# Kernel optimization log

Measured on AMD Instinct MI355X. Metric: run time of the kernel, lower is better.

The kernel has to match this reference:

```python
import jax, jax.numpy as jnp
import numpy as np

B, N, M, H, NH = 8, 1024, 512, 1024, 4
DH = H // NH          # 256 main attention head size
CDH = (H // 4) // 4   # 64  cross attention qk head size
EPS = 1e-12


def _ln(x, g, b):
    mu = jnp.mean(x, axis=-1, keepdims=True)
    var = jnp.mean((x - mu) ** 2, axis=-1, keepdims=True)
    return (x - mu) / jnp.sqrt(var + EPS) * g + b


def _heads(x, nh):
    b, n, d = x.shape
    return x.reshape(b, n, nh, d // nh).transpose(0, 2, 1, 3)  # [b,nh,n,dh]


def setup_inputs() -> dict:
    key = jax.random.key(0)
    ks = iter(jax.random.split(key, 64))
    nk = lambda: next(ks)
    w = lambda *s: jax.random.normal(nk(), s, jnp.float32) * 0.02
    inp = {}
    inp["hidden_states"] = jax.random.normal(nk(), (B, N, H), jnp.float32)
    inp["attention_mask"] = jnp.ones((B, N), jnp.float32)
    inp["structure_mask"] = (jax.random.uniform(nk(), (B, 3, N, N)) < 0.2).astype(jnp.float32)
    inp["Sentence_em"] = w(1, B, N, H)
    inp["entity_id_em"] = w(1, B, N, H)
    inp["cross_struct_mask"] = (jax.random.uniform(nk(), (B, 1, N, M)) < 0.3).astype(jnp.float32)
    inp["encoder_hidden_states"] = jax.random.normal(nk(), (1, B, M, H), jnp.float32)
    inp["encoder_attention_mask"] = jnp.ones((B, M), jnp.float32)
    # ---- Struct_SelfAttention params ----
    inp["Wq"] = w(H, 3 * DH); inp["bq"] = jnp.zeros(3 * DH)
    inp["Wk"] = w(H, 3 * DH); inp["bk"] = jnp.zeros(3 * DH)
    inp["Wv"] = w(H, H);      inp["bv"] = jnp.zeros(H)
    inp["Wq1"] = w(H, DH);    inp["bq1"] = jnp.zeros(DH)
    inp["Wk1"] = w(H, DH);    inp["bk1"] = jnp.zeros(DH)
    inp["ln_g"] = jnp.ones(H); inp["ln_b"] = jnp.zeros(H)
    inp["gnn_W"] = w(H, H); inp["gnn_b"] = jnp.zeros(H)
    inp["gnn_ln_g"] = jnp.ones(H); inp["gnn_ln_b"] = jnp.zeros(H)
    # ---- Cross_Attention params ----
    inp["cWq"] = w(H, H // 4); inp["cbq"] = jnp.zeros(H // 4)
    inp["cWk"] = w(H, H // 4); inp["cbk"] = jnp.zeros(H // 4)
    inp["cWv"] = w(H, H);      inp["cbv"] = jnp.zeros(H)
    inp["cWo"] = w(H, H);      inp["cbo"] = jnp.zeros(H)
    inp["cWg"] = w(2 * H, H);  inp["cbg"] = jnp.full((H,), -1.0, jnp.float32)  # Gate bias init -1
    inp["c_ln_g"] = jnp.ones(H); inp["c_ln_b"] = jnp.zeros(H)
    # ---- Output block params ----
    inp["oW1"] = w(H, H); inp["ob1"] = jnp.zeros(H)
    inp["o_ln1_g"] = jnp.ones(H); inp["o_ln1_b"] = jnp.zeros(H)
    inp["oW2"] = w(H, 2 * H); inp["ob2"] = jnp.zeros(2 * H)
    inp["oW3"] = w(2 * H, H); inp["ob3"] = jnp.zeros(H)
    inp["o_ln3_g"] = jnp.ones(H); inp["o_ln3_b"] = jnp.zeros(H)
    inp["layer_idx"] = 0
    return inp


def reference(hidden_states, attention_mask, structure_mask, Sentence_em, entity_id_em,
              cross_struct_mask, encoder_hidden_states, encoder_attention_mask,
              Wq, bq, Wk, bk, Wv, bv, Wq1, bq1, Wk1, bk1, ln_g, ln_b,
              gnn_W, gnn_b, gnn_ln_g, gnn_ln_b,
              cWq, cbq, cWk, cbk, cWv, cbv, cWo, cbo, cWg, cbg, c_ln_g, c_ln_b,
              oW1, ob1, o_ln1_g, o_ln1_b, oW2, ob2, oW3, ob3, o_ln3_g, o_ln3_b,
              layer_idx):
    hs = hidden_states
    q = _heads(hs @ Wq + bq, 3)          # [B,3,N,DH]
    k = _heads(hs @ Wk + bk, 3)
    v = _heads(hs @ Wv + bv, 4)          # [B,4,N,DH]
    s1 = jnp.einsum('bhnd,bhmd->bhnm', q, k)          # unscaled scores, 3 heads
    am0 = (1.0 - attention_mask)[:, None, None, :] * -10000.0
    s3 = s1 + am0
    # valid off-diagonal pairs mask (broadcasts over the 3 heads)
    pair = attention_mask[:, None, :, None] * attention_mask[:, None, None, :]
    idxw = ((pair * (1.0 - jnp.eye(N, dtype=jnp.float32))) > 0.5).astype(jnp.float32)  # [B,1,N,N]
    # sigmoid focal loss (gamma=2, alpha=0.25, mean over selected elements)
    p = jax.nn.sigmoid(s3)
    t = structure_mask
    fl = 0.25 * t * (1.0 - p) ** 2 * (-jax.nn.log_sigmoid(s3)) \
       + 0.75 * (1.0 - t) * p ** 2 * (-jax.nn.log_sigmoid(-s3))
    loss = jnp.sum(fl * idxw) / (3.0 * jnp.sum(idxw))
    # structural attention path (3 heads)
    s1 = s1 / np.float32(np.sqrt(DH)) + (1.0 - structure_mask) * -10000.0
    probs1 = jax.nn.softmax(s1, axis=-1)
    # positional/structural single-head path
    h1 = _ln(hs + Sentence_em[layer_idx] + entity_id_em[layer_idx], ln_g, ln_b)
    q1 = _heads(h1 @ Wq1 + bq1, 1)
    k1 = _heads(h1 @ Wk1 + bk1, 1)
    s2 = jnp.einsum('bhnd,bhmd->bhnm', q1, k1) / np.float32(np.sqrt(DH)) + am0
    probs2 = jax.nn.softmax(s2, axis=-1)
    probs = jnp.concatenate([probs2, probs1], axis=1)  # [B,4,N,N]
    ctx = jnp.einsum('bhnm,bhmd->bhnd', probs, v).transpose(0, 2, 1, 3).reshape(B, N, H)
    gnn_out = _ln(ctx @ gnn_W + gnn_b, gnn_ln_g, gnn_ln_b)
    # ---- Cross attention ----
    enc = encoder_hidden_states[layer_idx]            # [B,M,H]
    cq = _heads(gnn_out @ cWq + cbq, 4)               # [B,4,N,CDH]
    ck = _heads(enc @ cWk + cbk, 4)                   # [B,4,M,CDH]
    cv = _heads(enc @ cWv + cbv, 4)                   # [B,4,M,DH]
    cs = jnp.einsum('bhnd,bhmd->bhnm', cq, ck) / np.float32(np.sqrt(CDH))
    cs = cs + (1.0 - cross_struct_mask) * -10000.0
    cp = jax.nn.softmax(cs, axis=-1)
    cctx = jnp.einsum('bhnm,bhmd->bhnd', cp, cv).transpose(0, 2, 1, 3).reshape(B, N, H)
    cctx = cctx @ cWo + cbo
    gate = jax.nn.sigmoid(jnp.concatenate([gnn_out, cctx], axis=-1) @ cWg + cbg)
    cross_out = _ln(gate * cctx + (1.0 - gate) * gnn_out, c_ln_g, c_ln_b)
    # ---- Output block (gated FFN) ----
    h = _ln(cross_out @ oW1 + ob1 + hidden_states, o_ln1_g, o_ln1_b)
    h3 = jax.nn.gelu(h @ oW2 + ob2, approximate=False) @ oW3 + ob3
    out = _ln(h3 + h, o_ln3_g, o_ln3_b)
    return out, loss
```

## Files before the change

### kernel.cpp

```cpp
#include <hip/hip_runtime.h>
#include <math.h>

#define DEV __device__ __forceinline__

typedef short short8 __attribute__((ext_vector_type(8)));
typedef float float4v __attribute__((ext_vector_type(4)));

DEV unsigned short f2bf(float f) {
    union { float f; unsigned u; } v; v.f = f;
    unsigned r = v.u + 0x7FFFu + ((v.u >> 16) & 1u);
    return (unsigned short)(r >> 16);
}

DEV void async16(const unsigned short* g, unsigned short* l) {
    __builtin_amdgcn_global_load_lds(
        (const __attribute__((address_space(1))) unsigned int*)g,
        (__attribute__((address_space(3))) unsigned int*)l, 16, 0, 0);
}

DEV float block_reduce(float v, int mode) {
    #pragma unroll
    for (int off = 32; off; off >>= 1) {
        float o = __shfl_xor(v, off);
        v = mode ? fmaxf(v, o) : (v + o);
    }
    __shared__ float sbuf[4];
    __syncthreads();
    if ((threadIdx.x & 63) == 0) sbuf[threadIdx.x >> 6] = v;
    __syncthreads();
    float r = sbuf[0];
    #pragma unroll
    for (int w = 1; w < 4; w++) r = mode ? fmaxf(r, sbuf[w]) : (r + sbuf[w]);
    return r;
}

template <bool BIAS, bool ACCUM, bool GELU>
__global__ __launch_bounds__(256) void gemm_bf16_kernel(
    const unsigned short* __restrict__ A, int lda,
    const unsigned short* __restrict__ Bt, int ldb,
    const float* __restrict__ bias, const float* __restrict__ bias2,
    const float* __restrict__ bias3, int ns1, int ns2,
    float* __restrict__ Cf, unsigned short* __restrict__ Cb,
    int N, int K)
{
    __shared__ unsigned short As[128 * 32];
    __shared__ unsigned short Bs[128 * 32];
    const int tid = threadIdx.x;
    const int w = tid >> 6, lane = tid & 63;
    const int l15 = lane & 15, quad = lane >> 4;
    const int m0 = blockIdx.y * 128, n0 = blockIdx.x * 128;
    const int wm = (w >> 1) * 64, wn = (w & 1) * 64;
    const int lr = lane >> 2, lc = (lane & 3) * 8;

    float4v acc[4][4];
    #pragma unroll
    for (int i = 0; i < 4; i++)
        #pragma unroll
        for (int j = 0; j < 4; j++) acc[i][j] = (float4v){0.f, 0.f, 0.f, 0.f};

    const unsigned short* Ab = A  + (size_t)(m0 + w * 16 + lr) * lda + lc;
    const unsigned short* Bb = Bt + (size_t)(n0 + w * 16 + lr) * ldb + lc;
    unsigned short* AsW = As + (w * 16) * 32;
    unsigned short* BsW = Bs + (w * 16) * 32;

    for (int k0 = 0; k0 < K; k0 += 32) {
        __syncthreads();
        async16(Ab + k0, AsW);
        async16(Ab + (size_t)64 * lda + k0, AsW + 64 * 32);
        async16(Bb + k0, BsW);
        async16(Bb + (size_t)64 * ldb + k0, BsW + 64 * 32);
        __syncthreads();
        short8 Af[4], Bf[4];
        #pragma unroll
        for (int mt = 0; mt < 4; mt++)
            Af[mt] = *(const short8*)(As + (wm + mt * 16 + l15) * 32 + quad * 8);
        #pragma unroll
        for (int nt = 0; nt < 4; nt++)
            Bf[nt] = *(const short8*)(Bs + (wn + nt * 16 + l15) * 32 + quad * 8);
        #pragma unroll
        for (int mt = 0; mt < 4; mt++)
            #pragma unroll
            for (int nt = 0; nt < 4; nt++)
                acc[mt][nt] = __builtin_amdgcn_mfma_f32_16x16x32_bf16(
                    Af[mt], Bf[nt], acc[mt][nt], 0, 0, 0);
    }

    #pragma unroll
    for (int nt = 0; nt < 4; nt++) {
        const int n = n0 + wn + nt * 16 + l15;
        float bv = 0.f;
        if (BIAS) bv = (n < ns1) ? bias[n] : (n < ns2) ? bias2[n - ns1]
                                                       : bias3[n - ns2];
        #pragma unroll
        for (int mt = 0; mt < 4; mt++) {
            #pragma unroll
            for (int r = 0; r < 4; r++) {
                const int m = m0 + wm + mt * 16 + quad * 4 + r;
                const size_t off = (size_t)m * N + n;
                float v = acc[mt][nt][r] + bv;
                if (ACCUM) v += Cf[off];
                if (GELU) v = 0.5f * v * (1.f + erff(v * 0.70710678118654752f));
                if (Cf) Cf[off] = v;
                if (Cb) Cb[off] = f2bf(v);
            }
        }
    }
}

__global__ __launch_bounds__(256) void wtrans_kernel(
    const float* __restrict__ W, unsigned short* __restrict__ Wt, int K, int N)
{
    __shared__ float t[32][33];
    const int n0 = blockIdx.x * 32, k0 = blockIdx.y * 32;
    const int c = threadIdx.x & 31, r8 = threadIdx.x >> 5;
    #pragma unroll
    for (int i = 0; i < 4; i++) {
        const int r = r8 + i * 8;
        t[r][c] = W[(size_t)(k0 + r) * N + n0 + c];
    }
    __syncthreads();
    #pragma unroll
    for (int i = 0; i < 4; i++) {
        const int r = r8 + i * 8;
        Wt[(size_t)(n0 + r) * K + k0 + c] = f2bf(t[c][r]);
    }
}

__global__ __launch_bounds__(256) void trans_kernel(
    const unsigned short* __restrict__ v, unsigned short* __restrict__ Vt,
    int R, int C, int vpitch, int voff)
{
    __shared__ unsigned short t[32][33];
    const int b = blockIdx.z, r0 = blockIdx.x * 32, c0 = blockIdx.y * 32;
    const int c = threadIdx.x & 31, r8 = threadIdx.x >> 5;
    #pragma unroll
    for (int i = 0; i < 4; i++) {
        const int r = r8 + i * 8;
        t[r][c] = v[((size_t)b * R + r0 + r) * vpitch + voff + c0 + c];
    }
    __syncthreads();
    #pragma unroll
    for (int i = 0; i < 4; i++) {
        const int r = r8 + i * 8;
        Vt[((size_t)b * C + c0 + r) * R + r0 + c] = t[c][r];
    }
}

__global__ __launch_bounds__(256) void castbf_kernel(
    const float* __restrict__ x, unsigned short* __restrict__ y)
{
    const size_t i = ((size_t)blockIdx.x * 256 + threadIdx.x) * 4;
    float4 v = *(const float4*)(x + i);
    ushort4 o;
    o.x = f2bf(v.x); o.y = f2bf(v.y); o.z = f2bf(v.z); o.w = f2bf(v.w);
    *(ushort4*)(y + i) = o;
}

__global__ __launch_bounds__(256) void packmask_kernel(
    const float* __restrict__ x, unsigned int* __restrict__ bits)
{
    const size_t idx = (size_t)blockIdx.x * 256 + threadIdx.x;
    const unsigned long long m = __ballot(x[idx] > 0.5f);
    const int lane = threadIdx.x & 63;
    if (lane == 0)  bits[idx >> 5] = (unsigned)m;
    if (lane == 32) bits[idx >> 5] = (unsigned)(m >> 32);
}

DEV void ln_finish(float4 xv, const float* __restrict__ g,
                   const float* __restrict__ bb, float* __restrict__ outf,
                   unsigned short* __restrict__ outb, size_t base)
{
    float s  = xv.x + xv.y + xv.z + xv.w;
    float s2 = xv.x * xv.x + xv.y * xv.y + xv.z * xv.z + xv.w * xv.w;
    #pragma unroll
    for (int off = 32; off; off >>= 1) {
        s += __shfl_xor(s, off);
        s2 += __shfl_xor(s2, off);
    }
    __shared__ float sa[4], sb[4];
    if ((threadIdx.x & 63) == 0) {
        sa[threadIdx.x >> 6] = s; sb[threadIdx.x >> 6] = s2;
    }
    __syncthreads();
    s  = sa[0] + sa[1] + sa[2] + sa[3];
    s2 = sb[0] + sb[1] + sb[2] + sb[3];
    const float mu  = s * (1.f / 1024.f);
    const float var = fmaxf(s2 * (1.f / 1024.f) - mu * mu, 0.f);
    const float inv = rsqrtf(var + 1e-12f);
    const int tid = threadIdx.x;
    float4 gv = ((const float4*)g)[tid];
    float4 bv = ((const float4*)bb)[tid];
    float4 o;
    o.x = (xv.x - mu) * inv * gv.x + bv.x;
    o.y = (xv.y - mu) * inv * gv.y + bv.y;
    o.z = (xv.z - mu) * inv * gv.z + bv.z;
    o.w = (xv.w - mu) * inv * gv.w + bv.w;
    if (outf) ((float4*)(outf + base))[tid] = o;
    if (outb) {
        ushort4 ob;
        ob.x = f2bf(o.x); ob.y = f2bf(o.y); ob.z = f2bf(o.z); ob.w = f2bf(o.w);
        ((ushort4*)(outb + base))[tid] = ob;
    }
}

__global__ __launch_bounds__(256) void ln_kernel(
    const float* __restrict__ x, const float* __restrict__ r1,
    const float* __restrict__ r2, const float* __restrict__ g,
    const float* __restrict__ bb, float* __restrict__ outf,
    unsigned short* __restrict__ outb)
{
    const size_t base = (size_t)blockIdx.x * 1024;
    const int tid = threadIdx.x;
    float4 xv = ((const float4*)(x + base))[tid];
    if (r1) {
        float4 a = ((const float4*)(r1 + base))[tid];
        xv.x += a.x; xv.y += a.y; xv.z += a.z; xv.w += a.w;
    }
    if (r2) {
        float4 a = ((const float4*)(r2 + base))[tid];
        xv.x += a.x; xv.y += a.y; xv.z += a.z; xv.w += a.w;
    }
    ln_finish(xv, g, bb, outf, outb, base);
}

__global__ __launch_bounds__(256) void gate_ln_kernel(
    const float* __restrict__ gpre, const float* __restrict__ co,
    const float* __restrict__ gn, const float* __restrict__ g,
    const float* __restrict__ bb, float* __restrict__ outf,
    unsigned short* __restrict__ outb)
{
    const size_t base = (size_t)blockIdx.x * 1024;
    const int tid = threadIdx.x;
    float4 gp = ((const float4*)(gpre + base))[tid];
    float4 cv = ((const float4*)(co + base))[tid];
    float4 gv = ((const float4*)(gn + base))[tid];
    float4 xv; float s;
    s = 1.f / (1.f + __expf(-gp.x)); xv.x = s * cv.x + (1.f - s) * gv.x;
    s = 1.f / (1.f + __expf(-gp.y)); xv.y = s * cv.y + (1.f - s) * gv.y;
    s = 1.f / (1.f + __expf(-gp.z)); xv.z = s * cv.z + (1.f - s) * gv.z;
    s = 1.f / (1.f + __expf(-gp.w)); xv.w = s * cv.w + (1.f - s) * gv.w;
    ln_finish(xv, g, bb, outf, outb, base);
}

__global__ __launch_bounds__(256) void attn_mfma_kernel(
    const unsigned short* __restrict__ qkv,
    const unsigned short* __restrict__ q1k1,
    const unsigned short* __restrict__ Vt,
    const float* __restrict__ am,
    const unsigned int* __restrict__ smb,
    unsigned short* __restrict__ ctx,
    float* __restrict__ nump, float* __restrict__ denp)
{
    const int nb = blockIdx.x;
    const int h  = blockIdx.y >> 1;
    const int dh = blockIdx.y & 1;
    const int b  = blockIdx.z;
    const int tid = threadIdx.x;
    const int w = tid >> 6, lane = tid & 63;
    const int l15 = lane & 15, quad = lane >> 4;
    const int n0 = nb * 64;

    __shared__ unsigned short Ks[32 * 264];
    __shared__ unsigned short Vs[128 * 40];
    __shared__ unsigned short Ps[4][16 * 40];

    const unsigned short* qsrc; const unsigned short* ksrc; int pitch;
    if (h == 0) { qsrc = q1k1;                ksrc = q1k1 + 256;                pitch = 512; }
    else        { qsrc = qkv + (h - 1) * 256; ksrc = qkv + 768 + (h - 1) * 256; pitch = 2560; }

    short8 Qf[8];
    {
        const unsigned short* qrow =
            qsrc + (size_t)(b * 1024 + n0 + w * 16 + l15) * pitch;
        #pragma unroll
        for (int kk = 0; kk < 8; kk++)
            Qf[kk] = *(const short8*)(qrow + kk * 32 + quad * 8);
    }

    float4v O[8];
    #pragma unroll
    for (int i = 0; i < 8; i++) O[i] = (float4v){0.f, 0.f, 0.f, 0.f};
    float lsum[4] = {0.f, 0.f, 0.f, 0.f};
    float flsum = 0.f, dencnt = 0.f;
    const int nrow_base = n0 + w * 16 + quad * 4;
    const float* amrow = am + b * 1024;
    float amn[4];
    #pragma unroll
    for (int r = 0; r < 4; r++) amn[r] = amrow[nrow_base + r];
    const unsigned int* smw = (h > 0)
        ? smb + ((size_t)(b * 3 + (h - 1)) << 15) : nullptr;
    const int vrow0 = b * 1024 + h * 256 + dh * 128;

    for (int m0 = 0; m0 < 1024; m0 += 32) {
        __syncthreads();
        for (int c = tid; c < 1024; c += 256) {
            const int row = c >> 5, kc = (c & 31) * 8;
            *(uint4*)(Ks + row * 264 + kc) =
                *(const uint4*)(ksrc + (size_t)(b * 1024 + m0 + row) * pitch + kc);
        }
        for (int c = tid; c < 512; c += 256) {
            const int d = c >> 2, mc = (c & 3) * 8;
            *(uint4*)(Vs + d * 40 + mc) =
                *(const uint4*)(Vt + (size_t)(vrow0 + d) * 1024 + m0 + mc);
        }
        __syncthreads();

        float4v S[2];
        #pragma unroll
        for (int st = 0; st < 2; st++) {
            float4v a = (float4v){0.f, 0.f, 0.f, 0.f};
            #pragma unroll
            for (int kk = 0; kk < 8; kk++) {
                short8 Kf = *(const short8*)(Ks + (st * 16 + l15) * 264 + kk * 32 + quad * 8);
                a = __builtin_amdgcn_mfma_f32_16x16x32_bf16(Qf[kk], Kf, a, 0, 0, 0);
            }
            S[st] = a;
        }

        unsigned int wb[4];
        if (h > 0) {
            #pragma unroll
            for (int r = 0; r < 4; r++)
                wb[r] = smw[(size_t)(nrow_base + r) * 32 + (m0 >> 5)];
        }

        float e[2][4];
        #pragma unroll
        for (int st = 0; st < 2; st++) {
            const int mcol = m0 + st * 16 + l15;
            const float amm = amrow[mcol];
            const float am0 = (1.f - amm) * (-10000.f);
            #pragma unroll
            for (int r = 0; r < 4; r++) {
                const float sraw = S[st][r];
                float scv;
                if (h > 0) {
                    const float t = (float)((wb[r] >> (st * 16 + l15)) & 1u);
                    if (dh == 0) {
                        const int nrow = nrow_base + r;
                        const float s3 = sraw + am0;
                        const float idxw =
                            ((amn[r] * amm * ((mcol == nrow) ? 0.f : 1.f)) > 0.5f) ? 1.f : 0.f;
                        const float E = __expf(-fabsf(s3));
                        const float L = __logf(1.f + E);
                        const float R = 1.f / (1.f + E);
                        const float p = (s3 >= 0.f) ? R : E * R;
                        const float sp = fmaxf(s3, 0.f) + L;
                        const float omp = 1.f - p;
                        flsum += idxw * (0.25f * t * omp * omp * (sp - s3)
                                       + 0.75f * (1.f - t) * p * p * sp);
                        dencnt += idxw;
                    }
                    scv = sraw * 0.0625f + (1.f - t) * (-10000.f);
                } else {
                    scv = sraw * 0.0625f + am0;
                }
                const float ev = __expf(fminf(scv, 30.f));
                e[st][r] = ev;
                lsum[r] += ev;
            }
        }

        #pragma unroll
        for (int st = 0; st < 2; st++)
            #pragma unroll
            for (int r = 0; r < 4; r++)
                Ps[w][(quad * 4 + r) * 40 + st * 16 + l15] = f2bf(e[st][r]);
        const short8 Pf = *(const short8*)(&Ps[w][l15 * 40 + quad * 8]);
        #pragma unroll
        for (int dt = 0; dt < 8; dt++) {
            short8 Vf = *(const short8*)(Vs + (dt * 16 + l15) * 40 + quad * 8);
            O[dt] = __builtin_amdgcn_mfma_f32_16x16x32_bf16(Pf, Vf, O[dt], 0, 0, 0);
        }
    }

    float rinv[4];
    #pragma unroll
    for (int r = 0; r < 4; r++) {
        float s = lsum[r];
        #pragma unroll
        for (int off = 8; off; off >>= 1) s += __shfl_xor(s, off);
        rinv[r] = 1.f / s;
    }
    const int dcol0 = h * 256 + dh * 128;
    #pragma unroll
    for (int dt = 0; dt < 8; dt++)
        #pragma unroll
        for (int r = 0; r < 4; r++)
            ctx[(size_t)(b * 1024 + nrow_base + r) * 1024 + dcol0 + dt * 16 + l15]
                = f2bf(O[dt][r] * rinv[r]);

    if (h > 0 && dh == 0) {
        const float fb = block_reduce(flsum, 0);
        if (tid == 0) nump[(b * 3 + (h - 1)) * 16 + nb] = fb;
        if (h == 1) {
            const float db = block_reduce(dencnt, 0);
            if (tid == 0) denp[b * 16 + nb] = db;
        }
    }
}

__global__ __launch_bounds__(256) void cross_mfma_kernel(
    const unsigned short* __restrict__ cq,
    const unsigned short* __restrict__ ckv,
    const unsigned short* __restrict__ cvt,
    const unsigned int* __restrict__ csmb,
    unsigned short* __restrict__ cctx)
{
    const int nb = blockIdx.x;
    const int h  = blockIdx.y >> 1;
    const int dh = blockIdx.y & 1;
    const int b  = blockIdx.z;
    const int tid = threadIdx.x;
    const int w = tid >> 6, lane = tid & 63;
    const int l15 = lane & 15, quad = lane >> 4;
    const int n0 = nb * 64;

    __shared__ unsigned short Ks[32 * 72];
    __shared__ unsigned short Vs[128 * 40];
    __shared__ unsigned short Ps[4][16 * 40];

    short8 Qf[2];
    {
        const unsigned short* qrow =
            cq + (size_t)(b * 1024 + n0 + w * 16 + l15) * 256 + h * 64;
        #pragma unroll
        for (int kk = 0; kk < 2; kk++)
            Qf[kk] = *(const short8*)(qrow + kk * 32 + quad * 8);
    }

    float4v O[8];
    #pragma unroll
    for (int i = 0; i < 8; i++) O[i] = (float4v){0.f, 0.f, 0.f, 0.f};
    float lsum[4] = {0.f, 0.f, 0.f, 0.f};
    const int nrow_base = n0 + w * 16 + quad * 4;
    const unsigned int* csw = csmb + (size_t)(b * 1024) * 16;
    const int vrow0 = b * 1024 + h * 256 + dh * 128;

    for (int m0 = 0; m0 < 512; m0 += 32) {
        __syncthreads();
        {
            const int row = tid >> 3, kc = (tid & 7) * 8;
            *(uint4*)(Ks + row * 72 + kc) =
                *(const uint4*)(ckv + (size_t)(b * 512 + m0 + row) * 1280 + h * 64 + kc);
        }
        for (int c = tid; c < 512; c += 256) {
            const int d = c >> 2, mc = (c & 3) * 8;
            *(uint4*)(Vs + d * 40 + mc) =
                *(const uint4*)(cvt + (size_t)(vrow0 + d) * 512 + m0 + mc);
        }
        __syncthreads();

        float4v S[2];
        #pragma unroll
        for (int st = 0; st < 2; st++) {
            float4v a = (float4v){0.f, 0.f, 0.f, 0.f};
            #pragma unroll
            for (int kk = 0; kk < 2; kk++) {
                short8 Kf = *(const short8*)(Ks + (st * 16 + l15) * 72 + kk * 32 + quad * 8);
                a = __builtin_amdgcn_mfma_f32_16x16x32_bf16(Qf[kk], Kf, a, 0, 0, 0);
            }
            S[st] = a;
        }

        unsigned int wb[4];
        #pragma unroll
        for (int r = 0; r < 4; r++)
            wb[r] = csw[(size_t)(nrow_base + r) * 16 + (m0 >> 5)];

        float e[2][4];
        #pragma unroll
        for (int st = 0; st < 2; st++) {
            #pragma unroll
            for (int r = 0; r < 4; r++) {
                const float msk = (float)((wb[r] >> (st * 16 + l15)) & 1u);
                const float scv = S[st][r] * 0.125f + (1.f - msk) * (-10000.f);
                const float ev = __expf(fminf(scv, 30.f));
                e[st][r] = ev;
                lsum[r] += ev;
            }
        }

        #pragma unroll
        for (int st = 0; st < 2; st++)
            #pragma unroll
            for (int r = 0; r < 4; r++)
                Ps[w][(quad * 4 + r) * 40 + st * 16 + l15] = f2bf(e[st][r]);
        const short8 Pf = *(const short8*)(&Ps[w][l15 * 40 + quad * 8]);
        #pragma unroll
        for (int dt = 0; dt < 8; dt++) {
            short8 Vf = *(const short8*)(Vs + (dt * 16 + l15) * 40 + quad * 8);
            O[dt] = __builtin_amdgcn_mfma_f32_16x16x32_bf16(Pf, Vf, O[dt], 0, 0, 0);
        }
    }

    float rinv[4];
    #pragma unroll
    for (int r = 0; r < 4; r++) {
        float s = lsum[r];
        #pragma unroll
        for (int off = 8; off; off >>= 1) s += __shfl_xor(s, off);
        rinv[r] = 1.f / s;
    }
    const int dcol0 = h * 256 + dh * 128;
    #pragma unroll
    for (int dt = 0; dt < 8; dt++)
        #pragma unroll
        for (int r = 0; r < 4; r++)
            cctx[(size_t)(b * 1024 + nrow_base + r) * 1024 + dcol0 + dt * 16 + l15]
                = f2bf(O[dt][r] * rinv[r]);
}

__global__ __launch_bounds__(256) void loss_reduce_kernel(
    const float* __restrict__ nump, const float* __restrict__ denp,
    float* __restrict__ out)
{
    __shared__ double sn[256], sd[256];
    const int tid = threadIdx.x;
    double ns = 0.0, ds = 0.0;
    for (int i = tid; i < 384; i += 256) ns += (double)nump[i];
    for (int i = tid; i < 128; i += 256) ds += (double)denp[i];
    sn[tid] = ns; sd[tid] = ds;
    __syncthreads();
    for (int off = 128; off; off >>= 1) {
        if (tid < off) { sn[tid] += sn[tid + off]; sd[tid] += sd[tid + off]; }
        __syncthreads();
    }
    if (tid == 0) out[0] = (float)(sn[0] / (3.0 * sd[0]));
}

extern "C" void kernel_launch(void* const* d_in, const int* in_sizes, int n_in,
                              void* d_out, int out_size, void* d_ws, size_t ws_size,
                              hipStream_t stream)
{
    (void)in_sizes; (void)n_in; (void)out_size; (void)ws_size;
    const float* hs   = (const float*)d_in[0];
    const float* am   = (const float*)d_in[1];
    const float* smask= (const float*)d_in[2];
    const float* sent = (const float*)d_in[3];
    const float* ent  = (const float*)d_in[4];
    const float* csm  = (const float*)d_in[5];
    const float* enc  = (const float*)d_in[6];
    const float* Wq  = (const float*)d_in[8];  const float* bq  = (const float*)d_in[9];
    const float* Wk  = (const float*)d_in[10]; const float* bk  = (const float*)d_in[11];
    const float* Wv  = (const float*)d_in[12]; const float* bv  = (const float*)d_in[13];
    const float* Wq1 = (const float*)d_in[14]; const float* bq1 = (const float*)d_in[15];
    const float* Wk1 = (const float*)d_in[16]; const float* bk1 = (const float*)d_in[17];
    const float* ln_g= (const float*)d_in[18]; const float* ln_b= (const float*)d_in[19];
    const float* gW  = (const float*)d_in[20]; const float* gb  = (const float*)d_in[21];
    const float* gng = (const float*)d_in[22]; const float* gnb = (const float*)d_in[23];
    const float* cWq = (const float*)d_in[24]; const float* cbq = (const float*)d_in[25];
    const float* cWk = (const float*)d_in[26]; const float* cbk = (const float*)d_in[27];
    const float* cWv = (const float*)d_in[28]; const float* cbv = (const float*)d_in[29];
    const float* cWo = (const float*)d_in[30]; const float* cbo = (const float*)d_in[31];
    const float* cWg = (const float*)d_in[32]; const float* cbg = (const float*)d_in[33];
    const float* clg = (const float*)d_in[34]; const float* clb = (const float*)d_in[35];
    const float* oW1 = (const float*)d_in[36]; const float* ob1 = (const float*)d_in[37];
    const float* l1g = (const float*)d_in[38]; const float* l1b = (const float*)d_in[39];
    const float* oW2 = (const float*)d_in[40]; const float* ob2 = (const float*)d_in[41];
    const float* oW3 = (const float*)d_in[42]; const float* ob3 = (const float*)d_in[43];
    const float* l3g = (const float*)d_in[44]; const float* l3b = (const float*)d_in[45];
    float* out = (float*)d_out;

    typedef unsigned short ush;
    char* wsb = (char*)d_ws;
    ush* WT   = (ush*)wsb;
    ush* wqT  = WT;             ush* wkT  = WT + 786432;   ush* wvT  = WT + 1572864;
    ush* wq1T = WT + 2621440;   ush* wk1T = WT + 2883584;  ush* gWT_ = WT + 3145728;
    ush* cWqT = WT + 4194304;   ush* cWkT = WT + 4456448;  ush* cWvT = WT + 4718592;
    ush* cWoT = WT + 5767168;   ush* cWgT = WT + 6815744;  ush* oW1T = WT + 8912896;
    ush* oW2T = WT + 9961472;   ush* oW3T = WT + 12058624;
    (void)wkT; (void)wvT; (void)wk1T; (void)cWvT;
    ush*  hs_bf   = (ush*)(wsb + 28311552);
    ush*  enc_bf  = (ush*)(wsb + 45088768);
    ush*  qkv_bf  = (ush*)(wsb + 53477376);
    ush*  Vt      = (ush*)(wsb + 95420416);
    ush*  h1_bf   = (ush*)(wsb + 112197632);
    ush*  q1k1_bf = (ush*)(wsb + 128974848);
    ush*  ctx_bf  = (ush*)(wsb + 137363456);
    float* nump   = (float*)(wsb + 154140672);
    float* denp   = (float*)(wsb + 154142208);
    float* gnn_f  = (float*)(wsb + 154144768);
    float* gnnout_f = (float*)(wsb + 187699200);
    ush*  gnnout_b  = (ush*)(wsb + 221253632);
    unsigned int* smb  = (unsigned int*)(wsb + 187699200);
    unsigned int* csmb = (unsigned int*)(wsb + 28311552);
    ush*  cq_b      = (ush*)(wsb + 53477376);
    ush*  ckv_b     = (ush*)(wsb + 66060288);
    ush*  cctx_b    = (ush*)(wsb + 95420416);
    ush*  cvt       = (ush*)(wsb + 238030848);
    float* cctxo_f  = (float*)(wsb + 154144768);
    ush*  cctxo_b   = (ush*)(wsb + 28311552);
    float* gatepre_f= (float*)(wsb + 112197632);
    ush*  crossout_b= (ush*)(wsb + 221253632);
    float* t_f      = (float*)(wsb + 154144768);
    float* h_f      = (float*)(wsb + 187699200);
    ush*  h_b       = (ush*)(wsb + 28311552);
    ush*  h2g_b     = (ush*)(wsb + 45088768);
    float* h3_f     = (float*)(wsb + 154144768);

    const int BIG = 1 << 30;
    dim3 blk(256);
    castbf_kernel<<<8192, blk, 0, stream>>>(hs, hs_bf);
    castbf_kernel<<<4096, blk, 0, stream>>>(enc, enc_bf);
    packmask_kernel<<<98304, blk, 0, stream>>>(smask, smb);
    wtrans_kernel<<<dim3(768/32, 1024/32), blk, 0, stream>>>(Wq, wqT, 1024, 768);
    wtrans_kernel<<<dim3(768/32, 1024/32), blk, 0, stream>>>(Wk, wkT, 1024, 768);
    wtrans_kernel<<<dim3(32, 32), blk, 0, stream>>>(Wv, wvT, 1024, 1024);
    wtrans_kernel<<<dim3(8, 32), blk, 0, stream>>>(Wq1, wq1T, 1024, 256);
    wtrans_kernel<<<dim3(8, 32), blk, 0, stream>>>(Wk1, wk1T, 1024, 256);
    wtrans_kernel<<<dim3(32, 32), blk, 0, stream>>>(gW, gWT_, 1024, 1024);
    wtrans_kernel<<<dim3(8, 32), blk, 0, stream>>>(cWq, cWqT, 1024, 256);
    wtrans_kernel<<<dim3(8, 32), blk, 0, stream>>>(cWk, cWkT, 1024, 256);
    wtrans_kernel<<<dim3(32, 32), blk, 0, stream>>>(cWv, cWvT, 1024, 1024);
    wtrans_kernel<<<dim3(32, 32), blk, 0, stream>>>(cWo, cWoT, 1024, 1024);
    wtrans_kernel<<<dim3(32, 64), blk, 0, stream>>>(cWg, cWgT, 2048, 1024);
    wtrans_kernel<<<dim3(32, 32), blk, 0, stream>>>(oW1, oW1T, 1024, 1024);
    wtrans_kernel<<<dim3(64, 32), blk, 0, stream>>>(oW2, oW2T, 1024, 2048);
    wtrans_kernel<<<dim3(32, 64), blk, 0, stream>>>(oW3, oW3T, 2048, 1024);
    gemm_bf16_kernel<true,false,false><<<dim3(20, 64), blk, 0, stream>>>(
        hs_bf, 1024, wqT, 1024, bq, bk, bv, 768, 1536, nullptr, qkv_bf, 2560, 1024);
    packmask_kernel<<<16384, blk, 0, stream>>>(csm, csmb);
    ln_kernel<<<8192, blk, 0, stream>>>(hs, sent, ent, ln_g, ln_b, nullptr, h1_bf);
    gemm_bf16_kernel<true,false,false><<<dim3(4, 64), blk, 0, stream>>>(
        h1_bf, 1024, wq1T, 1024, bq1, bk1, nullptr, 256, BIG, nullptr, q1k1_bf, 512, 1024);
    trans_kernel<<<dim3(32, 32, 8), blk, 0, stream>>>(qkv_bf, Vt, 1024, 1024, 2560, 1536);
    attn_mfma_kernel<<<dim3(16, 8, 8), blk, 0, stream>>>(
        qkv_bf, q1k1_bf, Vt, am, smb, ctx_bf, nump, denp);
    loss_reduce_kernel<<<1, blk, 0, stream>>>(nump, denp, out + 8388608);
    gemm_bf16_kernel<true,false,false><<<dim3(8, 64), blk, 0, stream>>>(
        ctx_bf, 1024, gWT_, 1024, gb, nullptr, nullptr, BIG, BIG, gnn_f, nullptr, 1024, 1024);
    ln_kernel<<<8192, blk, 0, stream>>>(gnn_f, nullptr, nullptr, gng, gnb,
                                        gnnout_f, gnnout_b);
    gemm_bf16_kernel<true,false,false><<<dim3(2, 64), blk, 0, stream>>>(
        gnnout_b, 1024, cWqT, 1024, cbq, nullptr, nullptr, BIG, BIG, nullptr, cq_b, 256, 1024);
    gemm_bf16_kernel<true,false,false><<<dim3(10, 32), blk, 0, stream>>>(
        enc_bf, 1024, cWkT, 1024, cbk, cbv, nullptr, 256, BIG, nullptr, ckv_b, 1280, 1024);
    trans_kernel<<<dim3(16, 32, 8), blk, 0, stream>>>(ckv_b, cvt, 512, 1024, 1280, 256);
    cross_mfma_kernel<<<dim3(16, 8, 8), blk, 0, stream>>>(
        cq_b, ckv_b, cvt, csmb, cctx_b);
    gemm_bf16_kernel<true,false,false><<<dim3(8, 64), blk, 0, stream>>>(
        cctx_b, 1024, cWoT, 1024, cbo, nullptr, nullptr, BIG, BIG, cctxo_f, cctxo_b, 1024, 1024);
    gemm_bf16_kernel<true,false,false><<<dim3(8, 64), blk, 0, stream>>>(
        gnnout_b, 1024, cWgT, 2048, cbg, nullptr, nullptr, BIG, BIG, gatepre_f, nullptr, 1024, 1024);
    gemm_bf16_kernel<false,true,false><<<dim3(8, 64), blk, 0, stream>>>(
        cctxo_b, 1024, cWgT + 1024, 2048, nullptr, nullptr, nullptr, BIG, BIG, gatepre_f, nullptr, 1024, 1024);
    gate_ln_kernel<<<8192, blk, 0, stream>>>(gatepre_f, cctxo_f, gnnout_f,
                                             clg, clb, nullptr, crossout_b);
    gemm_bf16_kernel<true,false,false><<<dim3(8, 64), blk, 0, stream>>>(
        crossout_b, 1024, oW1T, 1024, ob1, nullptr, nullptr, BIG, BIG, t_f, nullptr, 1024, 1024);
    ln_kernel<<<8192, blk, 0, stream>>>(t_f, hs, nullptr, l1g, l1b, h_f, h_b);
    gemm_bf16_kernel<true,false,true><<<dim3(16, 64), blk, 0, stream>>>(
        h_b, 1024, oW2T, 1024, ob2, nullptr, nullptr, BIG, BIG, nullptr, h2g_b, 2048, 1024);
    gemm_bf16_kernel<true,false,false><<<dim3(8, 64), blk, 0, stream>>>(
        h2g_b, 2048, oW3T, 2048, ob3, nullptr, nullptr, BIG, BIG, h3_f, nullptr, 1024, 2048);
    ln_kernel<<<8192, blk, 0, stream>>>(h3_f, h_f, nullptr, l3g, l3b, out, nullptr);
}
```

Before: 1.329 ms.

## Cover full head dim per attention block, XCD-aware remap, fuse gate GEMMs via concat buffer

```diff
diff --git a/kernel.cpp b/kernel.cpp
--- a/kernel.cpp
+++ b/kernel.cpp
@@ -41,7 +41,7 @@
     const float* __restrict__ bias, const float* __restrict__ bias2,
     const float* __restrict__ bias3, int ns1, int ns2,
     float* __restrict__ Cf, unsigned short* __restrict__ Cb,
-    int N, int K)
+    int N, int Nb, int K)
 {
     __shared__ unsigned short As[128 * 32];
     __shared__ unsigned short Bs[128 * 32];
@@ -101,7 +101,7 @@
                 if (ACCUM) v += Cf[off];
                 if (GELU) v = 0.5f * v * (1.f + erff(v * 0.70710678118654752f));
                 if (Cf) Cf[off] = v;
-                if (Cb) Cb[off] = f2bf(v);
+                if (Cb) Cb[(size_t)m * Nb + n] = f2bf(v);
             }
         }
     }
@@ -168,7 +168,7 @@
 
 DEV void ln_finish(float4 xv, const float* __restrict__ g,
                    const float* __restrict__ bb, float* __restrict__ outf,
-                   unsigned short* __restrict__ outb, size_t base)
+                   unsigned short* __restrict__ outb, size_t base_f, size_t base_b)
 {
     float s  = xv.x + xv.y + xv.z + xv.w;
     float s2 = xv.x * xv.x + xv.y * xv.y + xv.z * xv.z + xv.w * xv.w;
@@ -195,11 +195,11 @@
     o.y = (xv.y - mu) * inv * gv.y + bv.y;
     o.z = (xv.z - mu) * inv * gv.z + bv.z;
     o.w = (xv.w - mu) * inv * gv.w + bv.w;
-    if (outf) ((float4*)(outf + base))[tid] = o;
+    if (outf) ((float4*)(outf + base_f))[tid] = o;
     if (outb) {
         ushort4 ob;
         ob.x = f2bf(o.x); ob.y = f2bf(o.y); ob.z = f2bf(o.z); ob.w = f2bf(o.w);
-        ((ushort4*)(outb + base))[tid] = ob;
+        ((ushort4*)(outb + base_b))[tid] = ob;
     }
 }
 
@@ -207,9 +207,10 @@
     const float* __restrict__ x, const float* __restrict__ r1,
     const float* __restrict__ r2, const float* __restrict__ g,
     const float* __restrict__ bb, float* __restrict__ outf,
-    unsigned short* __restrict__ outb)
+    unsigned short* __restrict__ outb, int obp)
 {
     const size_t base = (size_t)blockIdx.x * 1024;
+    const size_t base_b = (size_t)blockIdx.x * obp;
     const int tid = threadIdx.x;
     float4 xv = ((const float4*)(x + base))[tid];
     if (r1) {
@@ -220,7 +221,7 @@
         float4 a = ((const float4*)(r2 + base))[tid];
         xv.x += a.x; xv.y += a.y; xv.z += a.z; xv.w += a.w;
     }
-    ln_finish(xv, g, bb, outf, outb, base);
+    ln_finish(xv, g, bb, outf, outb, base, base_b);
 }
 
 __global__ __launch_bounds__(256) void gate_ln_kernel(
@@ -239,7 +240,7 @@
     s = 1.f / (1.f + __expf(-gp.y)); xv.y = s * cv.y + (1.f - s) * gv.y;
     s = 1.f / (1.f + __expf(-gp.z)); xv.z = s * cv.z + (1.f - s) * gv.z;
     s = 1.f / (1.f + __expf(-gp.w)); xv.w = s * cv.w + (1.f - s) * gv.w;
-    ln_finish(xv, g, bb, outf, outb, base);
+    ln_finish(xv, g, bb, outf, outb, base, base);
 }
 
 __global__ __launch_bounds__(256) void attn_mfma_kernel(
@@ -251,17 +252,18 @@
     unsigned short* __restrict__ ctx,
     float* __restrict__ nump, float* __restrict__ denp)
 {
-    const int nb = blockIdx.x;
-    const int h  = blockIdx.y >> 1;
-    const int dh = blockIdx.y & 1;
-    const int b  = blockIdx.z;
+    const int bid0 = blockIdx.x + 16 * blockIdx.y + 64 * blockIdx.z;
+    const int xcd = bid0 & 7, s = bid0 >> 3;
+    const int grp = xcd + 8 * (s >> 4);
+    const int nb = s & 15;
+    const int h = grp & 3, b = grp >> 2;
     const int tid = threadIdx.x;
     const int w = tid >> 6, lane = tid & 63;
     const int l15 = lane & 15, quad = lane >> 4;
     const int n0 = nb * 64;
 
     __shared__ unsigned short Ks[32 * 264];
-    __shared__ unsigned short Vs[128 * 40];
+    __shared__ unsigned short Vs[256 * 40];
     __shared__ unsigned short Ps[4][16 * 40];
 
     const unsigned short* qsrc; const unsigned short* ksrc; int pitch;
@@ -277,9 +279,9 @@
             Qf[kk] = *(const short8*)(qrow + kk * 32 + quad * 8);
     }
 
-    float4v O[8];
-    #pragma unroll
-    for (int i = 0; i < 8; i++) O[i] = (float4v){0.f, 0.f, 0.f, 0.f};
+    float4v O[16];
+    #pragma unroll
+    for (int i = 0; i < 16; i++) O[i] = (float4v){0.f, 0.f, 0.f, 0.f};
     float lsum[4] = {0.f, 0.f, 0.f, 0.f};
     float flsum = 0.f, dencnt = 0.f;
     const int nrow_base = n0 + w * 16 + quad * 4;
@@ -289,7 +291,7 @@
     for (int r = 0; r < 4; r++) amn[r] = amrow[nrow_base + r];
     const unsigned int* smw = (h > 0)
         ? smb + ((size_t)(b * 3 + (h - 1)) << 15) : nullptr;
-    const int vrow0 = b * 1024 + h * 256 + dh * 128;
+    const int vrow0 = b * 1024 + h * 256;
 
     for (int m0 = 0; m0 < 1024; m0 += 32) {
         __syncthreads();
@@ -298,7 +300,7 @@
             *(uint4*)(Ks + row * 264 + kc) =
                 *(const uint4*)(ksrc + (size_t)(b * 1024 + m0 + row) * pitch + kc);
         }
-        for (int c = tid; c < 512; c += 256) {
+        for (int c = tid; c < 1024; c += 256) {
             const int d = c >> 2, mc = (c & 3) * 8;
             *(uint4*)(Vs + d * 40 + mc) =
                 *(const uint4*)(Vt + (size_t)(vrow0 + d) * 1024 + m0 + mc);
@@ -336,21 +338,19 @@
                 float scv;
                 if (h > 0) {
                     const float t = (float)((wb[r] >> (st * 16 + l15)) & 1u);
-                    if (dh == 0) {
-                        const int nrow = nrow_base + r;
-                        const float s3 = sraw + am0;
-                        const float idxw =
-                            ((amn[r] * amm * ((mcol == nrow) ? 0.f : 1.f)) > 0.5f) ? 1.f : 0.f;
-                        const float E = __expf(-fabsf(s3));
-                        const float L = __logf(1.f + E);
-                        const float R = 1.f / (1.f + E);
-                        const float p = (s3 >= 0.f) ? R : E * R;
-                        const float sp = fmaxf(s3, 0.f) + L;
-                        const float omp = 1.f - p;
-                        flsum += idxw * (0.25f * t * omp * omp * (sp - s3)
-                                       + 0.75f * (1.f - t) * p * p * sp);
-                        dencnt += idxw;
-                    }
+                    const int nrow = nrow_base + r;
+                    const float s3 = sraw + am0;
+                    const float idxw =
+                        ((amn[r] * amm * ((mcol == nrow) ? 0.f : 1.f)) > 0.5f) ? 1.f : 0.f;
+                    const float E = __expf(-fabsf(s3));
+                    const float L = __logf(1.f + E);
+                    const float R = 1.f / (1.f + E);
+                    const float p = (s3 >= 0.f) ? R : E * R;
+                    const float sp = fmaxf(s3, 0.f) + L;
+                    const float omp = 1.f - p;
+                    flsum += idxw * (0.25f * t * omp * omp * (sp - s3)
+                                   + 0.75f * (1.f - t) * p * p * sp);
+                    dencnt += idxw;
                     scv = sraw * 0.0625f + (1.f - t) * (-10000.f);
                 } else {
                     scv = sraw * 0.0625f + am0;
@@ -368,7 +368,7 @@
                 Ps[w][(quad * 4 + r) * 40 + st * 16 + l15] = f2bf(e[st][r]);
         const short8 Pf = *(const short8*)(&Ps[w][l15 * 40 + quad * 8]);
         #pragma unroll
-        for (int dt = 0; dt < 8; dt++) {
+        for (int dt = 0; dt < 16; dt++) {
             short8 Vf = *(const short8*)(Vs + (dt * 16 + l15) * 40 + quad * 8);
             O[dt] = __builtin_amdgcn_mfma_f32_16x16x32_bf16(Pf, Vf, O[dt], 0, 0, 0);
         }
@@ -377,20 +377,19 @@
     float rinv[4];
     #pragma unroll
     for (int r = 0; r < 4; r++) {
-        float s = lsum[r];
-        #pragma unroll
-        for (int off = 8; off; off >>= 1) s += __shfl_xor(s, off);
-        rinv[r] = 1.f / s;
-    }
-    const int dcol0 = h * 256 + dh * 128;
-    #pragma unroll
-    for (int dt = 0; dt < 8; dt++)
+        float s2 = lsum[r];
+        #pragma unroll
+        for (int off = 8; off; off >>= 1) s2 += __shfl_xor(s2, off);
+        rinv[r] = 1.f / s2;
+    }
+    #pragma unroll
+    for (int dt = 0; dt < 16; dt++)
         #pragma unroll
         for (int r = 0; r < 4; r++)
-            ctx[(size_t)(b * 1024 + nrow_base + r) * 1024 + dcol0 + dt * 16 + l15]
+            ctx[(size_t)(b * 1024 + nrow_base + r) * 1024 + h * 256 + dt * 16 + l15]
                 = f2bf(O[dt][r] * rinv[r]);
 
-    if (h > 0 && dh == 0) {
+    if (h > 0) {
         const float fb = block_reduce(flsum, 0);
         if (tid == 0) nump[(b * 3 + (h - 1)) * 16 + nb] = fb;
         if (h == 1) {
@@ -407,17 +406,18 @@
     const unsigned int* __restrict__ csmb,
     unsigned short* __restrict__ cctx)
 {
-    const int nb = blockIdx.x;
-    const int h  = blockIdx.y >> 1;
-    const int dh = blockIdx.y & 1;
-    const int b  = blockIdx.z;
+    const int bid0 = blockIdx.x + 16 * blockIdx.y + 64 * blockIdx.z;
+    const int xcd = bid0 & 7, s = bid0 >> 3;
+    const int grp = xcd + 8 * (s >> 4);
+    const int nb = s & 15;
+    const int h = grp & 3, b = grp >> 2;
     const int tid = threadIdx.x;
     const int w = tid >> 6, lane = tid & 63;
     const int l15 = lane & 15, quad = lane >> 4;
     const int n0 = nb * 64;
 
     __shared__ unsigned short Ks[32 * 72];
-    __shared__ unsigned short Vs[128 * 40];
+    __shared__ unsigned short Vs[256 * 40];
     __shared__ unsigned short Ps[4][16 * 40];
 
     short8 Qf[2];
@@ -429,13 +429,13 @@
             Qf[kk] = *(const short8*)(qrow + kk * 32 + quad * 8);
     }
 
-    float4v O[8];
-    #pragma unroll
-    for (int i = 0; i < 8; i++) O[i] = (float4v){0.f, 0.f, 0.f, 0.f};
+    float4v O[16];
+    #pragma unroll
+    for (int i = 0; i < 16; i++) O[i] = (float4v){0.f, 0.f, 0.f, 0.f};
     float lsum[4] = {0.f, 0.f, 0.f, 0.f};
     const int nrow_base = n0 + w * 16 + quad * 4;
     const unsigned int* csw = csmb + (size_t)(b * 1024) * 16;
-    const int vrow0 = b * 1024 + h * 256 + dh * 128;
+    const int vrow0 = b * 1024 + h * 256;
 
     for (int m0 = 0; m0 < 512; m0 += 32) {
         __syncthreads();
@@ -444,7 +444,7 @@
             *(uint4*)(Ks + row * 72 + kc) =
                 *(const uint4*)(ckv + (size_t)(b * 512 + m0 + row) * 1280 + h * 64 + kc);
         }
-        for (int c = tid; c < 512; c += 256) {
+        for (int c = tid; c < 1024; c += 256) {
             const int d = c >> 2, mc = (c & 3) * 8;
             *(uint4*)(Vs + d * 40 + mc) =
                 *(const uint4*)(cvt + (size_t)(vrow0 + d) * 512 + m0 + mc);
@@ -488,7 +488,7 @@
                 Ps[w][(quad * 4 + r) * 40 + st * 16 + l15] = f2bf(e[st][r]);
         const short8 Pf = *(const short8*)(&Ps[w][l15 * 40 + quad * 8]);
         #pragma unroll
-        for (int dt = 0; dt < 8; dt++) {
+        for (int dt = 0; dt < 16; dt++) {
             short8 Vf = *(const short8*)(Vs + (dt * 16 + l15) * 40 + quad * 8);
             O[dt] = __builtin_amdgcn_mfma_f32_16x16x32_bf16(Pf, Vf, O[dt], 0, 0, 0);
         }
@@ -497,17 +497,16 @@
     float rinv[4];
     #pragma unroll
     for (int r = 0; r < 4; r++) {
-        float s = lsum[r];
-        #pragma unroll
-        for (int off = 8; off; off >>= 1) s += __shfl_xor(s, off);
-        rinv[r] = 1.f / s;
-    }
-    const int dcol0 = h * 256 + dh * 128;
-    #pragma unroll
-    for (int dt = 0; dt < 8; dt++)
+        float s2 = lsum[r];
+        #pragma unroll
+        for (int off = 8; off; off >>= 1) s2 += __shfl_xor(s2, off);
+        rinv[r] = 1.f / s2;
+    }
+    #pragma unroll
+    for (int dt = 0; dt < 16; dt++)
         #pragma unroll
         for (int r = 0; r < 4; r++)
-            cctx[(size_t)(b * 1024 + nrow_base + r) * 1024 + dcol0 + dt * 16 + l15]
+            cctx[(size_t)(b * 1024 + nrow_base + r) * 1024 + h * 256 + dt * 16 + l15]
                 = f2bf(O[dt][r] * rinv[r]);
 }
 
@@ -582,16 +581,15 @@
     float* denp   = (float*)(wsb + 154142208);
     float* gnn_f  = (float*)(wsb + 154144768);
     float* gnnout_f = (float*)(wsb + 187699200);
-    ush*  gnnout_b  = (ush*)(wsb + 221253632);
     unsigned int* smb  = (unsigned int*)(wsb + 187699200);
     unsigned int* csmb = (unsigned int*)(wsb + 28311552);
+    ush*  gc_b      = (ush*)(wsb + 112197632);
     ush*  cq_b      = (ush*)(wsb + 53477376);
     ush*  ckv_b     = (ush*)(wsb + 66060288);
     ush*  cctx_b    = (ush*)(wsb + 95420416);
     ush*  cvt       = (ush*)(wsb + 238030848);
     float* cctxo_f  = (float*)(wsb + 154144768);
-    ush*  cctxo_b   = (ush*)(wsb + 28311552);
-    float* gatepre_f= (float*)(wsb + 112197632);
+    float* gatepre_f= (float*)(wsb + 45088768);
     ush*  crossout_b= (ush*)(wsb + 221253632);
     float* t_f      = (float*)(wsb + 154144768);
     float* h_f      = (float*)(wsb + 187699200);
@@ -619,40 +617,38 @@
     wtrans_kernel<<<dim3(64, 32), blk, 0, stream>>>(oW2, oW2T, 1024, 2048);
     wtrans_kernel<<<dim3(32, 64), blk, 0, stream>>>(oW3, oW3T, 2048, 1024);
     gemm_bf16_kernel<true,false,false><<<dim3(20, 64), blk, 0, stream>>>(
-        hs_bf, 1024, wqT, 1024, bq, bk, bv, 768, 1536, nullptr, qkv_bf, 2560, 1024);
+        hs_bf, 1024, wqT, 1024, bq, bk, bv, 768, 1536, nullptr, qkv_bf, 2560, 2560, 1024);
     packmask_kernel<<<16384, blk, 0, stream>>>(csm, csmb);
-    ln_kernel<<<8192, blk, 0, stream>>>(hs, sent, ent, ln_g, ln_b, nullptr, h1_bf);
+    ln_kernel<<<8192, blk, 0, stream>>>(hs, sent, ent, ln_g, ln_b, nullptr, h1_bf, 1024);
     gemm_bf16_kernel<true,false,false><<<dim3(4, 64), blk, 0, stream>>>(
-        h1_bf, 1024, wq1T, 1024, bq1, bk1, nullptr, 256, BIG, nullptr, q1k1_bf, 512, 1024);
+        h1_bf, 1024, wq1T, 1024, bq1, bk1, nullptr, 256, BIG, nullptr, q1k1_bf, 512, 512, 1024);
     trans_kernel<<<dim3(32, 32, 8), blk, 0, stream>>>(qkv_bf, Vt, 1024, 1024, 2560, 1536);
-    attn_mfma_kernel<<<dim3(16, 8, 8), blk, 0, stream>>>(
+    attn_mfma_kernel<<<dim3(16, 4, 8), blk, 0, stream>>>(
         qkv_bf, q1k1_bf, Vt, am, smb, ctx_bf, nump, denp);
     loss_reduce_kernel<<<1, blk, 0, stream>>>(nump, denp, out + 8388608);
     gemm_bf16_kernel<true,false,false><<<dim3(8, 64), blk, 0, stream>>>(
-        ctx_bf, 1024, gWT_, 1024, gb, nullptr, nullptr, BIG, BIG, gnn_f, nullptr, 1024, 1024);
+        ctx_bf, 1024, gWT_, 1024, gb, nullptr, nullptr, BIG, BIG, gnn_f, nullptr, 1024, 1024, 1024);
     ln_kernel<<<8192, blk, 0, stream>>>(gnn_f, nullptr, nullptr, gng, gnb,
-                                        gnnout_f, gnnout_b);
+                                        gnnout_f, gc_b, 2048);
     gemm_bf16_kernel<true,false,false><<<dim3(2, 64), blk, 0, stream>>>(
-        gnnout_b, 1024, cWqT, 1024, cbq, nullptr, nullptr, BIG, BIG, nullptr, cq_b, 256, 1024);
+        gc_b, 2048, cWqT, 1024, cbq, nullptr, nullptr, BIG, BIG, nullptr, cq_b, 256, 256, 1024);
     gemm_bf16_kernel<true,false,false><<<dim3(10, 32), blk, 0, stream>>>(
-        enc_bf, 1024, cWkT, 1024, cbk, cbv, nullptr, 256, BIG, nullptr, ckv_b, 1280, 1024);
+        enc_bf, 1024, cWkT, 1024, cbk, cbv, nullptr, 256, BIG, nullptr, ckv_b, 1280, 1280, 1024);
     trans_kernel<<<dim3(16, 32, 8), blk, 0, stream>>>(ckv_b, cvt, 512, 1024, 1280, 256);
-    cross_mfma_kernel<<<dim3(16, 8, 8), blk, 0, stream>>>(
+    cross_mfma_kernel<<<dim3(16, 4, 8), blk, 0, stream>>>(
         cq_b, ckv_b, cvt, csmb, cctx_b);
     gemm_bf16_kernel<true,false,false><<<dim3(8, 64), blk, 0, stream>>>(
-        cctx_b, 1024, cWoT, 1024, cbo, nullptr, nullptr, BIG, BIG, cctxo_f, cctxo_b, 1024, 1024);
+        cctx_b, 1024, cWoT, 1024, cbo, nullptr, nullptr, BIG, BIG, cctxo_f, gc_b + 1024, 1024, 2048, 1024);
     gemm_bf16_kernel<true,false,false><<<dim3(8, 64), blk, 0, stream>>>(
-        gnnout_b, 1024, cWgT, 2048, cbg, nullptr, nullptr, BIG, BIG, gatepre_f, nullptr, 1024, 1024);
-    gemm_bf16_kernel<false,true,false><<<dim3(8, 64), blk, 0, stream>>>(
-        cctxo_b, 1024, cWgT + 1024, 2048, nullptr, nullptr, nullptr, BIG, BIG, gatepre_f, nullptr, 1024, 1024);
+        gc_b, 2048, cWgT, 2048, cbg, nullptr, nullptr, BIG, BIG, gatepre_f, nullptr, 1024, 1024, 2048);
     gate_ln_kernel<<<8192, blk, 0, stream>>>(gatepre_f, cctxo_f, gnnout_f,
                                              clg, clb, nullptr, crossout_b);
     gemm_bf16_kernel<true,false,false><<<dim3(8, 64), blk, 0, stream>>>(
-        crossout_b, 1024, oW1T, 1024, ob1, nullptr, nullptr, BIG, BIG, t_f, nullptr, 1024, 1024);
-    ln_kernel<<<8192, blk, 0, stream>>>(t_f, hs, nullptr, l1g, l1b, h_f, h_b);
+        crossout_b, 1024, oW1T, 1024, ob1, nullptr, nullptr, BIG, BIG, t_f, nullptr, 1024, 1024, 1024);
+    ln_kernel<<<8192, blk, 0, stream>>>(t_f, hs, nullptr, l1g, l1b, h_f, h_b, 1024);
     gemm_bf16_kernel<true,false,true><<<dim3(16, 64), blk, 0, stream>>>(
-        h_b, 1024, oW2T, 1024, ob2, nullptr, nullptr, BIG, BIG, nullptr, h2g_b, 2048, 1024);
+        h_b, 1024, oW2T, 1024, ob2, nullptr, nullptr, BIG, BIG, nullptr, h2g_b, 2048, 2048, 1024);
     gemm_bf16_kernel<true,false,false><<<dim3(8, 64), blk, 0, stream>>>(
-        h2g_b, 2048, oW3T, 2048, ob3, nullptr, nullptr, BIG, BIG, h3_f, nullptr, 1024, 2048);
-    ln_kernel<<<8192, blk, 0, stream>>>(h3_f, h_f, nullptr, l3g, l3b, out, nullptr);
-}
+        h2g_b, 2048, oW3T, 2048, ob3, nullptr, nullptr, BIG, BIG, h3_f, nullptr, 1024, 1024, 2048);
+    ln_kernel<<<8192, blk, 0, stream>>>(h3_f, h_f, nullptr, l3g, l3b, out, nullptr, 1024);
+}
```

After: 1.207 ms. -9.2%, faster.
